# Performance work log

Hardware: AMD Instinct MI355X
Metric: run time of the kernel (lower is better)

The kernel has to match this reference:

```python
import jax, jax.numpy as jnp
import numpy as np

D_IN = 2
D_Q = 8
N_TOKEN = 512
FPD = 64            # fre_per_dim = (N_TOKEN*D_Q)**(1/D_IN)
FRE_UB = 10.0
FFN_MULT = 4
N_ATTN = 4
N_MLP = 2           # n_total_blocks - n_attn_blocks
B = 8192
EPS_LN = 1e-5
EPS_SIG = 1e-8


def _ln(x, g, b):
    m = jnp.mean(x, axis=-1, keepdims=True)
    v = jnp.var(x, axis=-1, keepdims=True)
    return (x - m) * jax.lax.rsqrt(v + EPS_LN) * g + b


def _rff_buffers():
    # freqs: linspace(0, fre_ub, FPD+1)[1:]
    f = jnp.linspace(0.0, FRE_UB, FPD + 1)[1:]
    # cartesian_prod(f, f): first factor varies slowest
    grid = jnp.stack(jnp.meshgrid(f, f, indexing='ij'), axis=-1).reshape(-1, D_IN)
    omega_raw = grid.reshape(N_TOKEN, D_Q, D_IN)
    G = omega_raw[..., -1]                                 # [T, d_q]
    f_min = G.min(axis=-1, keepdims=True)
    f_max = G.max(axis=-1, keepdims=True)
    G = (G - f_min) / (f_max - f_min + EPS_SIG) * 2.0 - 1.0
    omega = omega_raw * jnp.sqrt(jnp.asarray(2.0 / (D_Q * N_TOKEN), jnp.float32))
    phase = jnp.linspace(0.0, 2.0 * np.pi, N_TOKEN * D_Q).reshape(1, N_TOKEN, D_Q)
    return omega.astype(jnp.float32), G.astype(jnp.float32), phase.astype(jnp.float32)


def setup_inputs() -> dict:
    key = jax.random.key(0)
    ks = iter(jax.random.split(key, 64))
    T, F = N_TOKEN, FFN_MULT * N_TOKEN
    s = 0.02

    def w(shape):
        return (jax.random.normal(next(ks), shape, jnp.float32) * s)

    omega, G, phase = _rff_buffers()
    inp = {
        'x': jax.random.normal(next(ks), (B, D_IN), jnp.float32),
        'omega': omega, 'G': G, 'phase': phase,
        'l1_w': w((T, D_IN)), 'l1_b': jnp.zeros((T,), jnp.float32),
        # attention blocks (stacked over N_ATTN)
        'mu_w': w((N_ATTN, T, T)), 'mu_b': jnp.zeros((N_ATTN, T), jnp.float32),
        'sg_w': w((N_ATTN, T, T)), 'sg_b': jnp.zeros((N_ATTN, T), jnp.float32),
        'aln_q_g': jnp.ones((N_ATTN, T), jnp.float32), 'aln_q_b': jnp.zeros((N_ATTN, T), jnp.float32),
        'aln_f_g': jnp.ones((N_ATTN, T), jnp.float32), 'aln_f_b': jnp.zeros((N_ATTN, T), jnp.float32),
        'a_w1': w((N_ATTN, F, T)), 'a_b1': jnp.zeros((N_ATTN, F), jnp.float32),
        'a_w2': w((N_ATTN, T, F)), 'a_b2': jnp.zeros((N_ATTN, T), jnp.float32),
        # MLP blocks (stacked over N_MLP)
        'mln_g': jnp.ones((N_MLP, T), jnp.float32), 'mln_b': jnp.zeros((N_MLP, T), jnp.float32),
        'm_w1': w((N_MLP, F, T)), 'm_b1': jnp.zeros((N_MLP, F), jnp.float32),
        'm_w2': w((N_MLP, T, F)), 'm_b2': jnp.zeros((N_MLP, T), jnp.float32),
        'ro_w': w((1, T)), 'ro_b': jnp.zeros((1,), jnp.float32),
    }
    return inp


def reference(x, omega, G, phase, l1_w, l1_b, mu_w, mu_b, sg_w, sg_b,
              aln_q_g, aln_q_b, aln_f_g, aln_f_b, a_w1, a_b1, a_w2, a_b2,
              mln_g, mln_b, m_w1, m_b1, m_w2, m_b2, ro_w, ro_b):
    # RFF tokenizer: H[b,n,k] = cos(omega[n,k,:] . x[b,:] + phase)
    H = jnp.cos(jnp.einsum('nkd,bd->bnk', omega, x) + phase)   # [B,T,d_q]
    Q = jax.nn.silu(x @ l1_w.T + l1_b)                          # [B,T]
    for i in range(N_ATTN):
        q = _ln(Q, aln_q_g[i], aln_q_b[i])
        mu = jnp.tanh(q @ mu_w[i].T + mu_b[i])[..., None]       # [B,T,1]
        sig = (q @ sg_w[i].T + sg_b[i])[..., None]              # [B,T,1]
        # Gaussian kernelized pseudo-attention; G broadcasts [T,d_q] -> [B,T,d_q]
        S = jnp.exp(-0.5 * (G - mu) ** 2 / (sig * sig + EPS_SIG))
        Q = Q + jnp.sum(S * H, axis=-1)
        h = _ln(Q, aln_f_g[i], aln_f_b[i])
        Q = Q + jax.nn.silu(h @ a_w1[i].T + a_b1[i]) @ a_w2[i].T + a_b2[i]
    for i in range(N_MLP):
        h = _ln(Q, mln_g[i], mln_b[i])
        Q = Q + jax.nn.silu(h @ m_w1[i].T + m_b1[i]) @ m_w2[i].T + m_b2[i]
    out = jax.nn.silu(Q) @ ro_w.T + ro_b                        # [B,1]
    return out[:, 0]
```

## Files before the change

kernel.cpp:

```cpp
#include <hip/hip_runtime.h>
#include <cmath>

namespace {

constexpr int BB = 8192;
constexpr int TT = 512;
constexpr int FF = 2048;
constexpr float EPS_LN  = 1e-5f;
constexpr float EPS_SIG = 1e-8f;

typedef _Float16 half8 __attribute__((ext_vector_type(8)));
typedef _Float16 half4 __attribute__((ext_vector_type(4)));
typedef float f32x4 __attribute__((ext_vector_type(4)));

typedef __attribute__((address_space(1))) void gvoid_t;
typedef __attribute__((address_space(3))) void lvoid_t;

__device__ __forceinline__ void async16(void* lds, const void* g) {
    __builtin_amdgcn_global_load_lds((gvoid_t*)g, (lvoid_t*)lds, 16, 0, 0);
}

__device__ __forceinline__ float silu_f(float v) {
    return v / (1.0f + expf(-v));
}
__device__ __forceinline__ float silu_fast(float v) {
    return v * __builtin_amdgcn_rcpf(1.0f + __expf(-v));
}

template <bool LO>
__global__ __launch_bounds__(256) void cvt_kernel(
    const float* __restrict__ s, _Float16* __restrict__ hi,
    _Float16* __restrict__ lo, int n) {
    int i = (blockIdx.x * 256 + threadIdx.x) * 4;
    if (i >= n) return;
    float4 v = *(const float4*)(s + i);
    half4 h;
    h[0] = (_Float16)v.x; h[1] = (_Float16)v.y;
    h[2] = (_Float16)v.z; h[3] = (_Float16)v.w;
    *(half4*)(hi + i) = h;
    if (LO) {
        half4 l;
        l[0] = (_Float16)(v.x - (float)h[0]);
        l[1] = (_Float16)(v.y - (float)h[1]);
        l[2] = (_Float16)(v.z - (float)h[2]);
        l[3] = (_Float16)(v.w - (float)h[3]);
        *(half4*)(lo + i) = l;
    }
}

__global__ __launch_bounds__(256) void cvtcat_kernel(
    const float* __restrict__ s, _Float16* __restrict__ hi,
    _Float16* __restrict__ lo, int base) {
    int i = (blockIdx.x * 256 + threadIdx.x) * 4;
    int dst = ((i >> 18) << 19) + base + (i & 262143);
    float4 v = *(const float4*)(s + i);
    half4 h, l;
    h[0] = (_Float16)v.x; h[1] = (_Float16)v.y;
    h[2] = (_Float16)v.z; h[3] = (_Float16)v.w;
    l[0] = (_Float16)(v.x - (float)h[0]);
    l[1] = (_Float16)(v.y - (float)h[1]);
    l[2] = (_Float16)(v.z - (float)h[2]);
    l[3] = (_Float16)(v.w - (float)h[3]);
    *(half4*)(hi + dst) = h;
    *(half4*)(lo + dst) = l;
}

__global__ __launch_bounds__(256) void tok_kernel(
    const float* __restrict__ x, const float* __restrict__ l1w,
    const float* __restrict__ l1b, float* __restrict__ Q) {
    int idx = blockIdx.x * 256 + threadIdx.x;
    int b = idx >> 9, t = idx & 511;
    float x0 = x[2 * b], x1 = x[2 * b + 1];
    float v = fmaf(x0, l1w[2 * t], fmaf(x1, l1w[2 * t + 1], l1b[t]));
    Q[idx] = silu_f(v);
}

template <bool LO>
__global__ __launch_bounds__(256) void ln_kernel(
    const float* __restrict__ X, const float* __restrict__ g,
    const float* __restrict__ bia, _Float16* __restrict__ Y,
    _Float16* __restrict__ Ylo) {
    int lane = threadIdx.x & 63;
    int row  = blockIdx.x * 4 + (threadIdx.x >> 6);
    const float* xr = X + (size_t)row * TT;
    float v[8];
    {
        float4 a = *(const float4*)(xr + lane * 8);
        float4 c = *(const float4*)(xr + lane * 8 + 4);
        v[0]=a.x; v[1]=a.y; v[2]=a.z; v[3]=a.w;
        v[4]=c.x; v[5]=c.y; v[6]=c.z; v[7]=c.w;
    }
    float s = 0.f;
    #pragma unroll
    for (int i = 0; i < 8; ++i) s += v[i];
    #pragma unroll
    for (int off = 32; off > 0; off >>= 1) s += __shfl_down(s, off);
    float mean = __shfl(s, 0) * (1.0f / TT);
    float ss = 0.f;
    #pragma unroll
    for (int i = 0; i < 8; ++i) { float d = v[i] - mean; ss = fmaf(d, d, ss); }
    #pragma unroll
    for (int off = 32; off > 0; off >>= 1) ss += __shfl_down(ss, off);
    float var  = __shfl(ss, 0) * (1.0f / TT);
    float rstd = rsqrtf(var + EPS_LN);
    half8 hv, lv;
    #pragma unroll
    for (int i = 0; i < 8; ++i) {
        int t = lane * 8 + i;
        float o = (v[i] - mean) * rstd * g[t] + bia[t];
        hv[i] = (_Float16)o;
        if (LO) lv[i] = (_Float16)(o - (float)hv[i]);
    }
    *(half8*)(Y + (size_t)row * TT + lane * 8) = hv;
    if (LO) *(half8*)(Ylo + (size_t)row * TT + lane * 8) = lv;
}

template <int BM, int BN, int WGM, int WGN, int NBUF, bool SPLIT, int ACT,
          bool RESID, typename OutT>
__global__ __launch_bounds__(WGM * WGN * 64) void gemmdp_kernel(
    const _Float16* __restrict__ A, const _Float16* __restrict__ Alo,
    const _Float16* __restrict__ W, const _Float16* __restrict__ Wlo,
    const float* __restrict__ bias, const float* __restrict__ bias2,
    const float* __restrict__ R, OutT* __restrict__ C,
    int N, int K, int nsplit) {
    constexpr int BK      = 32;
    constexpr int THREADS = WGM * WGN * 64;
    constexpr int NS   = SPLIT ? 2 : 1;
    constexpr int D    = NBUF - 1;
    constexpr int CH_A = NS * BM * 4;
    constexpr int CH_T = NS * (BM + BN) * 4;
    constexpr int LPT  = CH_T / THREADS;
    static_assert(CH_T % THREADS == 0 && CH_A % THREADS == 0, "staging split");
    constexpr int ABUF = NS * BM * BK;
    constexpr int WBUF = NS * BN * BK;
    constexpr int WOFF = NBUF * ABUF;
    constexpr int WTM  = BM / WGM;
    constexpr int WTN  = BN / WGN;
    constexpr int MI   = WTM / 16;
    constexpr int NI   = WTN / 16;

    __shared__ alignas(16) _Float16 lds[NBUF * (ABUF + WBUF)];

    const int tid = threadIdx.x;
    const int m0  = blockIdx.x * BM;
    const int n0  = blockIdx.y * BN;

    const _Float16* Asrc[2] = {A, Alo};
    const _Float16* Wsrc[2] = {W, Wlo};

    const _Float16* gsrc[LPT];
    int off0[LPT], bstr[LPT];
    #pragma unroll
    for (int j = 0; j < LPT; ++j) {
        int idx = j * THREADS + tid;
        if (j * THREADS < CH_A) {
            int s   = idx / (BM * 4);
            int rc  = idx % (BM * 4);
            int row = rc >> 2, sl = rc & 3;
            int src = sl ^ ((row >> 1) & 3);
            gsrc[j] = Asrc[s] + (size_t)(m0 + row) * K + src * 8;
            off0[j] = (s * BM + row) * BK + sl * 8;
            bstr[j] = ABUF;
        } else {
            int i2  = idx - CH_A;
            int s   = i2 / (BN * 4);
            int rc  = i2 % (BN * 4);
            int row = rc >> 2, sl = rc & 3;
            int src = sl ^ ((row >> 1) & 3);
            gsrc[j] = Wsrc[s] + (size_t)(n0 + row) * K + src * 8;
            off0[j] = WOFF + (s * BN + row) * BK + sl * 8;
            bstr[j] = WBUF;
        }
    }

    auto stage = [&](int buf, int k0) {
        #pragma unroll
        for (int j = 0; j < LPT; ++j)
            async16(&lds[off0[j] + buf * bstr[j]], gsrc[j] + k0);
    };

    const int wid  = tid >> 6;
    const int wr   = wid / WGN;
    const int wc   = wid % WGN;
    const int lane = tid & 63;
    const int fr   = lane & 15;
    const int q    = lane >> 4;
    const int swz  = (q ^ ((fr >> 1) & 3)) * 8;

    const f32x4 vzero = {0.f, 0.f, 0.f, 0.f};
    f32x4 acc[MI][NI];
    #pragma unroll
    for (int mi = 0; mi < MI; ++mi)
        #pragma unroll
        for (int ni = 0; ni < NI; ++ni) acc[mi][ni] = vzero;

    auto body = [&](int buf) {
        const int da = buf * ABUF;
        const int dw = WOFF + buf * WBUF;
        half8 a[NS][MI], b[NS][NI];
        #pragma unroll
        for (int s = 0; s < NS; ++s) {
            #pragma unroll
            for (int mi = 0; mi < MI; ++mi)
                a[s][mi] = *(const half8*)&lds[da + (s * BM + wr * WTM + mi * 16 + fr) * BK + swz];
            #pragma unroll
            for (int ni = 0; ni < NI; ++ni)
                b[s][ni] = *(const half8*)&lds[dw + (s * BN + wc * WTN + ni * 16 + fr) * BK + swz];
        }
        __builtin_amdgcn_s_setprio(1);
        #pragma unroll
        for (int mi = 0; mi < MI; ++mi)
            #pragma unroll
            for (int ni = 0; ni < NI; ++ni)
                acc[mi][ni] = __builtin_amdgcn_mfma_f32_16x16x32_f16(
                    a[0][mi], b[0][ni], acc[mi][ni], 0, 0, 0);
        if (SPLIT) {
            #pragma unroll
            for (int mi = 0; mi < MI; ++mi)
                #pragma unroll
                for (int ni = 0; ni < NI; ++ni)
                    acc[mi][ni] = __builtin_amdgcn_mfma_f32_16x16x32_f16(
                        a[1][mi], b[0][ni], acc[mi][ni], 0, 0, 0);
            #pragma unroll
            for (int mi = 0; mi < MI; ++mi)
                #pragma unroll
                for (int ni = 0; ni < NI; ++ni)
                    acc[mi][ni] = __builtin_amdgcn_mfma_f32_16x16x32_f16(
                        a[0][mi], b[1][ni], acc[mi][ni], 0, 0, 0);
        }
        __builtin_amdgcn_s_setprio(0);
    };

    const int NK = K / BK;

    #pragma unroll
    for (int s = 0; s < D; ++s) stage(s, s * BK);

    int rbuf = 0, sbuf = D;
    for (int ki = 0; ki < NK - D; ++ki) {
        asm volatile("s_waitcnt vmcnt(%0)" :: "n"((D - 1) * LPT) : "memory");
        __builtin_amdgcn_s_barrier();
        asm volatile("" ::: "memory");
        stage(sbuf, (ki + D) * BK);
        sbuf = (sbuf + 1 == NBUF) ? 0 : sbuf + 1;
        body(rbuf);
        rbuf = (rbuf + 1 == NBUF) ? 0 : rbuf + 1;
    }
    if constexpr (D >= 3) {
        asm volatile("s_waitcnt vmcnt(%0)" :: "n"(2 * LPT) : "memory");
        __builtin_amdgcn_s_barrier();
        asm volatile("" ::: "memory");
        body(rbuf);
        rbuf = (rbuf + 1 == NBUF) ? 0 : rbuf + 1;
    }
    if constexpr (D >= 2) {
        asm volatile("s_waitcnt vmcnt(%0)" :: "n"(1 * LPT) : "memory");
        __builtin_amdgcn_s_barrier();
        asm volatile("" ::: "memory");
        body(rbuf);
        rbuf = (rbuf + 1 == NBUF) ? 0 : rbuf + 1;
    }
    asm volatile("s_waitcnt vmcnt(0)" ::: "memory");
    __builtin_amdgcn_s_barrier();
    asm volatile("" ::: "memory");
    body(rbuf);

    const bool fh = (n0 < nsplit);
    const float* bp = fh ? bias : bias2;
    const int coff = fh ? 0 : nsplit;
    const int r0 = q * 4;
    #pragma unroll
    for (int mi = 0; mi < MI; ++mi) {
        #pragma unroll
        for (int ni = 0; ni < NI; ++ni) {
            const int col = n0 + wc * WTN + ni * 16 + fr;
            const float bv = bp[col - coff];
            #pragma unroll
            for (int r = 0; r < 4; ++r) {
                const int row = m0 + wr * WTM + mi * 16 + r0 + r;
                float v = acc[mi][ni][r] + bv;
                if (ACT == 1) v = silu_fast(v);
                if (ACT == 3 && fh) v = tanhf(v);
                if (RESID) v += R[(size_t)row * N + col];
                C[(size_t)row * N + col] = (OutT)v;
            }
        }
    }
}

__global__ __launch_bounds__(256) void attn_kernel(
    float* __restrict__ Q, const float* __restrict__ MS,
    const float* __restrict__ x,
    const float* __restrict__ omega, const float* __restrict__ G,
    const float* __restrict__ phase) {
    __shared__ float cs[8][260];
    __shared__ float gs[8][260];
    const int tid = threadIdx.x;
    const int b   = blockIdx.x >> 1;
    const int t0  = (blockIdx.x & 1) * 256;
    const float x0 = x[2 * b], x1 = x[2 * b + 1];
    #pragma unroll
    for (int it = 0; it < 8; ++it) {
        int j = it * 256 + tid;
        int e = t0 * 8 + j;
        float2 om = *(const float2*)(omega + 2 * e);
        float arg = fmaf(om.x, x0, fmaf(om.y, x1, phase[e]));
        cs[j & 7][j >> 3] = __cosf(arg);
        gs[j & 7][j >> 3] = G[e];
    }
    __syncthreads();
    const int t   = t0 + tid;
    const int idx = blockIdx.x * 256 + tid;
    float mu  = MS[(size_t)b * 1024 + t];
    float sig = MS[(size_t)b * 1024 + 512 + t];
    float inv = -0.5f * __builtin_amdgcn_rcpf(fmaf(sig, sig, EPS_SIG));
    float acc = 0.f;
    #pragma unroll
    for (int k = 0; k < 8; ++k) {
        float d = gs[k][tid] - mu;
        acc = fmaf(__expf(d * d * inv), cs[k][tid], acc);
    }
    Q[idx] += acc;
}

__global__ __launch_bounds__(256) void readout_kernel(
    const float* __restrict__ Q, const float* __restrict__ row_,
    const float* __restrict__ rob, float* __restrict__ out) {
    int lane = threadIdx.x & 63;
    int row  = blockIdx.x * 4 + (threadIdx.x >> 6);
    const float* qr = Q + (size_t)row * TT;
    float acc = 0.f;
    #pragma unroll
    for (int i = 0; i < 8; ++i) {
        int t = lane * 8 + i;
        acc = fmaf(silu_f(qr[t]), row_[t], acc);
    }
    #pragma unroll
    for (int off = 32; off > 0; off >>= 1) acc += __shfl_down(acc, off);
    if (lane == 0) out[row] = acc + rob[0];
}

}

extern "C" void kernel_launch(void* const* d_in, const int* in_sizes, int n_in,
                              void* d_out, int out_size, void* d_ws, size_t ws_size,
                              hipStream_t stream) {
    const float* x     = (const float*)d_in[0];
    const float* omega = (const float*)d_in[1];
    const float* G     = (const float*)d_in[2];
    const float* phase = (const float*)d_in[3];
    const float* l1_w  = (const float*)d_in[4];
    const float* l1_b  = (const float*)d_in[5];
    const float* mu_w  = (const float*)d_in[6];
    const float* mu_b  = (const float*)d_in[7];
    const float* sg_w  = (const float*)d_in[8];
    const float* sg_b  = (const float*)d_in[9];
    const float* alqg  = (const float*)d_in[10];
    const float* alqb  = (const float*)d_in[11];
    const float* alfg  = (const float*)d_in[12];
    const float* alfb  = (const float*)d_in[13];
    const float* a_w1  = (const float*)d_in[14];
    const float* a_b1  = (const float*)d_in[15];
    const float* a_w2  = (const float*)d_in[16];
    const float* a_b2  = (const float*)d_in[17];
    const float* mln_g = (const float*)d_in[18];
    const float* mln_b = (const float*)d_in[19];
    const float* m_w1  = (const float*)d_in[20];
    const float* m_b1  = (const float*)d_in[21];
    const float* m_w2  = (const float*)d_in[22];
    const float* m_b2  = (const float*)d_in[23];
    const float* ro_w  = (const float*)d_in[24];
    const float* ro_b  = (const float*)d_in[25];

    char* ws = (char*)d_ws;
    float*     Q    = (float*)ws;
    _Float16*  h_hi = (_Float16*)(ws + 16777216);
    _Float16*  h_lo = (_Float16*)(ws + 25165824);
    _Float16*  mid  = (_Float16*)(ws + 33554432);
    float*     MS   = (float*)(ws + 33554432);
    _Float16*  wbuf = (_Float16*)(ws + 67108864);

    _Float16* msw_hi = wbuf;
    _Float16* msw_lo = msw_hi + 2097152;
    _Float16* aw1    = msw_lo + 2097152;
    _Float16* aw2    = aw1 + 4194304;
    _Float16* mw1    = aw2 + 4194304;
    _Float16* mw2    = mw1 + 2097152;

    dim3 blk(256);
    const int BIG = 1 << 30;

    cvtcat_kernel<<<1024, blk, 0, stream>>>(mu_w, msw_hi, msw_lo, 0);
    cvtcat_kernel<<<1024, blk, 0, stream>>>(sg_w, msw_hi, msw_lo, 262144);
    cvt_kernel<false><<<4096, blk, 0, stream>>>(a_w1, aw1, nullptr, 4194304);
    cvt_kernel<false><<<4096, blk, 0, stream>>>(a_w2, aw2, nullptr, 4194304);
    cvt_kernel<false><<<2048, blk, 0, stream>>>(m_w1, mw1, nullptr, 2097152);
    cvt_kernel<false><<<2048, blk, 0, stream>>>(m_w2, mw2, nullptr, 2097152);

    tok_kernel<<<BB * TT / 256, blk, 0, stream>>>(x, l1_w, l1_b, Q);

    for (int i = 0; i < 4; ++i) {
        ln_kernel<true><<<BB / 4, blk, 0, stream>>>(
            Q, alqg + i * TT, alqb + i * TT, h_hi, h_lo);
        gemmdp_kernel<256, 128, 2, 4, 3, true, 3, false, float>
            <<<dim3(BB / 256, 1024 / 128), dim3(512), 0, stream>>>(
            h_hi, h_lo, msw_hi + (size_t)i * 524288, msw_lo + (size_t)i * 524288,
            mu_b + i * TT, sg_b + i * TT, nullptr, MS, 1024, TT, TT);
        attn_kernel<<<BB * TT / 256, blk, 0, stream>>>(Q, MS, x, omega, G, phase);
        ln_kernel<false><<<BB / 4, blk, 0, stream>>>(
            Q, alfg + i * TT, alfb + i * TT, h_hi, nullptr);
        gemmdp_kernel<256, 256, 2, 4, 4, false, 1, false, _Float16>
            <<<dim3(BB / 256, FF / 256), dim3(512), 0, stream>>>(
            h_hi, nullptr, aw1 + (size_t)i * 1048576, nullptr,
            a_b1 + i * FF, a_b1 + i * FF, nullptr, mid, FF, TT, BIG);
        gemmdp_kernel<128, 128, 2, 2, 4, false, 0, true, float>
            <<<dim3(BB / 128, TT / 128), dim3(256), 0, stream>>>(
            mid, nullptr, aw2 + (size_t)i * 1048576, nullptr,
            a_b2 + i * TT, a_b2 + i * TT, Q, Q, TT, FF, BIG);
    }
    for (int i = 0; i < 2; ++i) {
        ln_kernel<false><<<BB / 4, blk, 0, stream>>>(
            Q, mln_g + i * TT, mln_b + i * TT, h_hi, nullptr);
        gemmdp_kernel<256, 256, 2, 4, 4, false, 1, false, _Float16>
            <<<dim3(BB / 256, FF / 256), dim3(512), 0, stream>>>(
            h_hi, nullptr, mw1 + (size_t)i * 1048576, nullptr,
            m_b1 + i * FF, m_b1 + i * FF, nullptr, mid, FF, TT, BIG);
        gemmdp_kernel<128, 128, 2, 2, 4, false, 0, true, float>
            <<<dim3(BB / 128, TT / 128), dim3(256), 0, stream>>>(
            mid, nullptr, mw2 + (size_t)i * 1048576, nullptr,
            m_b2 + i * TT, m_b2 + i * TT, Q, Q, TT, FF, BIG);
    }

    readout_kernel<<<BB / 4, blk, 0, stream>>>(Q, ro_w, ro_b, (float*)d_out);
}
```

Measured before the change: 811.3 us.

## Fuse attention update with following LayerNorm and widen down-projection GEMM warps

New measurement: 784.8 us. 1.03x faster.

```diff
diff --git a/kernel.cpp b/kernel.cpp
--- a/kernel.cpp
+++ b/kernel.cpp
@@ -288,39 +288,62 @@
     }
 }
 
-__global__ __launch_bounds__(256) void attn_kernel(
+__global__ __launch_bounds__(512) void attnln_kernel(
     float* __restrict__ Q, const float* __restrict__ MS,
     const float* __restrict__ x,
     const float* __restrict__ omega, const float* __restrict__ G,
-    const float* __restrict__ phase) {
-    __shared__ float cs[8][260];
-    __shared__ float gs[8][260];
+    const float* __restrict__ phase,
+    const float* __restrict__ g, const float* __restrict__ bia,
+    _Float16* __restrict__ Y) {
+    __shared__ float cs[8][516];
+    __shared__ float gs[8][516];
+    __shared__ float red[2][8];
     const int tid = threadIdx.x;
-    const int b   = blockIdx.x >> 1;
-    const int t0  = (blockIdx.x & 1) * 256;
+    const int b   = blockIdx.x;
     const float x0 = x[2 * b], x1 = x[2 * b + 1];
     #pragma unroll
     for (int it = 0; it < 8; ++it) {
-        int j = it * 256 + tid;
-        int e = t0 * 8 + j;
-        float2 om = *(const float2*)(omega + 2 * e);
-        float arg = fmaf(om.x, x0, fmaf(om.y, x1, phase[e]));
+        int j = it * 512 + tid;
+        float2 om = *(const float2*)(omega + 2 * j);
+        float arg = fmaf(om.x, x0, fmaf(om.y, x1, phase[j]));
         cs[j & 7][j >> 3] = __cosf(arg);
-        gs[j & 7][j >> 3] = G[e];
+        gs[j & 7][j >> 3] = G[j];
     }
     __syncthreads();
-    const int t   = t0 + tid;
-    const int idx = blockIdx.x * 256 + tid;
+    const int t = tid;
     float mu  = MS[(size_t)b * 1024 + t];
     float sig = MS[(size_t)b * 1024 + 512 + t];
     float inv = -0.5f * __builtin_amdgcn_rcpf(fmaf(sig, sig, EPS_SIG));
     float acc = 0.f;
     #pragma unroll
     for (int k = 0; k < 8; ++k) {
-        float d = gs[k][tid] - mu;
-        acc = fmaf(__expf(d * d * inv), cs[k][tid], acc);
-    }
-    Q[idx] += acc;
+        float d = gs[k][t] - mu;
+        acc = fmaf(__expf(d * d * inv), cs[k][t], acc);
+    }
+    const size_t idx = (size_t)b * TT + t;
+    float qn = Q[idx] + acc;
+    Q[idx] = qn;
+    const int wid = tid >> 6, lane = tid & 63;
+    float s = qn;
+    #pragma unroll
+    for (int off = 32; off > 0; off >>= 1) s += __shfl_down(s, off);
+    if (lane == 0) red[0][wid] = s;
+    __syncthreads();
+    float tot = 0.f;
+    #pragma unroll
+    for (int w = 0; w < 8; ++w) tot += red[0][w];
+    float mean = tot * (1.0f / TT);
+    float d = qn - mean;
+    float ss = d * d;
+    #pragma unroll
+    for (int off = 32; off > 0; off >>= 1) ss += __shfl_down(ss, off);
+    if (lane == 0) red[1][wid] = ss;
+    __syncthreads();
+    float vtot = 0.f;
+    #pragma unroll
+    for (int w = 0; w < 8; ++w) vtot += red[1][w];
+    float rstd = rsqrtf(vtot * (1.0f / TT) + EPS_LN);
+    Y[idx] = (_Float16)(d * rstd * g[t] + bia[t]);
 }
 
 __global__ __launch_bounds__(256) void readout_kernel(
@@ -406,15 +429,14 @@
             <<<dim3(BB / 256, 1024 / 128), dim3(512), 0, stream>>>(
             h_hi, h_lo, msw_hi + (size_t)i * 524288, msw_lo + (size_t)i * 524288,
             mu_b + i * TT, sg_b + i * TT, nullptr, MS, 1024, TT, TT);
-        attn_kernel<<<BB * TT / 256, blk, 0, stream>>>(Q, MS, x, omega, G, phase);
-        ln_kernel<false><<<BB / 4, blk, 0, stream>>>(
-            Q, alfg + i * TT, alfb + i * TT, h_hi, nullptr);
+        attnln_kernel<<<BB, dim3(512), 0, stream>>>(
+            Q, MS, x, omega, G, phase, alfg + i * TT, alfb + i * TT, h_hi);
         gemmdp_kernel<256, 256, 2, 4, 4, false, 1, false, _Float16>
             <<<dim3(BB / 256, FF / 256), dim3(512), 0, stream>>>(
             h_hi, nullptr, aw1 + (size_t)i * 1048576, nullptr,
             a_b1 + i * FF, a_b1 + i * FF, nullptr, mid, FF, TT, BIG);
-        gemmdp_kernel<128, 128, 2, 2, 4, false, 0, true, float>
-            <<<dim3(BB / 128, TT / 128), dim3(256), 0, stream>>>(
+        gemmdp_kernel<128, 128, 2, 4, 4, false, 0, true, float>
+            <<<dim3(BB / 128, TT / 128), dim3(512), 0, stream>>>(
             mid, nullptr, aw2 + (size_t)i * 1048576, nullptr,
             a_b2 + i * TT, a_b2 + i * TT, Q, Q, TT, FF, BIG);
     }
@@ -425,8 +447,8 @@
             <<<dim3(BB / 256, FF / 256), dim3(512), 0, stream>>>(
             h_hi, nullptr, mw1 + (size_t)i * 1048576, nullptr,
             m_b1 + i * FF, m_b1 + i * FF, nullptr, mid, FF, TT, BIG);
-        gemmdp_kernel<128, 128, 2, 2, 4, false, 0, true, float>
-            <<<dim3(BB / 128, TT / 128), dim3(256), 0, stream>>>(
+        gemmdp_kernel<128, 128, 2, 4, 4, false, 0, true, float>
+            <<<dim3(BB / 128, TT / 128), dim3(512), 0, stream>>>(
             mid, nullptr, mw2 + (size_t)i * 1048576, nullptr,
             m_b2 + i * TT, m_b2 + i * TT, Q, Q, TT, FF, BIG);
     }
```
